# Performance work log

Measured on AMD Instinct MI355X. Metric: run time of the kernel, lower is better.

Reference implementation:

```python
import jax, jax.numpy as jnp
import numpy as np

# ---- static config (matches init_kwargs) ----
OC, IC, K, S, PAD = 128, 64, 3, 1, 1
M, T, R = 5, 8, 2.5            # ALSH m, table_size, LSH bucket width r
SPAN = K * K * IC              # kernel_span = 576


def setup_inputs() -> dict:
    key = jax.random.key(0)
    k1, k2, k3, k4 = jax.random.split(key, 4)
    # xavier_uniform on the (OC, SPAN) kernel matrix
    bound = float(np.sqrt(6.0 / (OC + SPAN)))
    kernels = jax.random.uniform(k1, (OC, SPAN), minval=-bound, maxval=bound, dtype=jnp.float32)
    a = jax.random.normal(k2, (SPAN + M,), dtype=jnp.float32)          # LSH projection
    b = jax.random.uniform(k3, (), minval=0.0, maxval=R, dtype=jnp.float32)  # LSH offset
    x = jax.random.normal(k4, (16, IC, 56, 56), dtype=jnp.float32)
    return {"x": x, "kernels": kernels, "a": a, "b": b, "mode": 0}


def _im2col(x):
    # [B, SPAN, H2, W2] with feature order (C, kh, kw)
    p = jax.lax.conv_general_dilated_patches(x, (K, K), (S, S), [(PAD, PAD), (PAD, PAD)])
    B, _, H2, W2 = p.shape
    # patch matrix [SPAN, B*H2*W2]
    return p.transpose(1, 0, 2, 3).reshape(SPAN, -1), B, H2, W2


def _bucket(h):
    # floor((h+b)/r); fmod table_size; abs  (matches torch .fmod_ then .abs_)
    return jnp.abs(jnp.fmod(h.astype(jnp.int32), T))


def reference(x, kernels, a, b, mode):
    patch_matr, B, H2, W2 = _im2col(x)            # [SPAN, N], N = B*H2*W2

    # ---- vote: hash every patch column with Q-augmentation (append m halves) ----
    v = a[:SPAN] @ patch_matr + 0.5 * jnp.sum(a[SPAN:])      # [N]
    votes = _bucket(jnp.floor((v + b) / R))
    counts = jnp.zeros((T,), jnp.int32).at[votes].add(1)
    bucket = jnp.argmax(counts)                               # most common bucket

    # ---- hash table: hash each kernel row with P-augmentation (norm powers) ----
    norms2 = jnp.sum(kernels * kernels, axis=1)               # ||k||^2, [OC]
    powers = jnp.stack([norms2 ** (2 ** i) for i in range(M)], axis=1)  # ||k||^{2,4,...,2^M}
    hk = kernels @ a[:SPAN] + powers @ a[SPAN:]               # [OC]
    kidx = _bucket(jnp.floor((hk + b) / R))                   # bucket of each kernel

    # ---- select kernels in the winning bucket; scale by |rows|/OC ----
    mask = (kidx == bucket).astype(x.dtype)                   # [OC]
    cnt = jnp.sum(mask)
    # original gathers the selected rows (variable oc); we scatter back to the
    # full OC channels (zeros for inactive kernels) for static shapes.
    # empty bucket -> dense conv with all kernels, no rescale.
    factor = jnp.where(cnt > 0, mask * (OC / jnp.maximum(cnt, 1.0)), jnp.ones_like(mask))

    out = (kernels * factor[:, None]) @ patch_matr            # [OC, N]
    out = out.reshape(OC, B, H2 * W2).transpose(1, 0, 2)
    return out.reshape(B, OC, H2, W2)
```

## Files before the change

### kernel.cpp

```cpp
#include <hip/hip_runtime.h>
#include <math.h>

#define IC 64
#define OC 128
#define HH 56
#define WW 56
#define BATCH 16
#define HP 58
#define HW (HH*WW)
#define NPIX (BATCH*HW)
#define SPAN 576
#define TSIZE 8
#define PADBLK 211
#define VBANDS 28
#define VBLOCKS (BATCH*VBANDS)
#define NBLK1 (PADBLK + VBLOCKS + OC)

typedef unsigned short ushort_t;
typedef unsigned int uint_t;
typedef __attribute__((ext_vector_type(8))) __bf16 bf16x8;
typedef __attribute__((ext_vector_type(4))) float f32x4;

__device__ __forceinline__ ushort_t bf16_rne(float f) {
  uint_t u = __builtin_bit_cast(uint_t, f);
  u += 0x7FFFu + ((u >> 16) & 1u);
  return (ushort_t)(u >> 16);
}

__global__ __launch_bounds__(256)
void prep_kernel(const float* __restrict__ x, const float* __restrict__ kernels,
                 const float* __restrict__ a, const float* __restrict__ bptr,
                 ushort_t* __restrict__ xpad, ushort_t* __restrict__ w2,
                 int* __restrict__ rbucket, int* __restrict__ hist_partial) {
  __shared__ float tl[224 * 9];
  __shared__ int hist[TSIZE];
  __shared__ float red0[256], red1[256];
  const int bx = blockIdx.x, t = threadIdx.x;

  if (bx < PADBLK) {
    int idx = bx * 256 + t;
    if (idx >= BATCH * HP * HP) return;
    int b = idx / (HP * HP);
    int rem = idx % (HP * HP);
    int y = rem / HP, xw = rem % HP;
    int h = y - 1, w = xw - 1;
    bool inb = ((unsigned)h < (unsigned)HH) && ((unsigned)w < (unsigned)WW);
    const float* src = x + (size_t)b * IC * HW + (inb ? h * WW + w : 0);
    uint_t* dst = (uint_t*)(xpad + (size_t)idx * IC);
    #pragma unroll
    for (int c2 = 0; c2 < IC / 2; ++c2) {
      float f0 = inb ? src[(2 * c2) * HW] : 0.0f;
      float f1 = inb ? src[(2 * c2 + 1) * HW] : 0.0f;
      dst[c2] = (uint_t)bf16_rne(f0) | ((uint_t)bf16_rne(f1) << 16);
    }
  } else if (bx < PADBLK + VBLOCKS) {
    const int vb = bx - PADBLK;
    const int b = vb / VBANDS, band = vb % VBANDS;
    const int r0 = band * 2;
    if (t < TSIZE) hist[t] = 0;
    if (t < 224) {
      int prow = r0 - 1 + t / 56;
      int col = t % 56;
      float t9[9] = {0, 0, 0, 0, 0, 0, 0, 0, 0};
      if ((unsigned)prow < (unsigned)HH) {
        const float* xb = x + (size_t)b * IC * HW + prow * WW + col;
        #pragma unroll
        for (int c = 0; c < IC; ++c) {
          float xv = xb[(size_t)c * HW];
          #pragma unroll
          for (int tap = 0; tap < 9; ++tap) t9[tap] += a[c * 9 + tap] * xv;
        }
      }
      #pragma unroll
      for (int tap = 0; tap < 9; ++tap) tl[t * 9 + tap] = t9[tap];
    }
    __syncthreads();
    if (t < 112) {
      int lr = t / 56;
      int col = t % 56;
      float v = 0.0f;
      #pragma unroll
      for (int kh = 0; kh < 3; ++kh) {
        int gr = r0 + lr - 1 + kh;
        #pragma unroll
        for (int kw = 0; kw < 3; ++kw) {
          int cc = col - 1 + kw;
          if ((unsigned)gr < (unsigned)HH && (unsigned)cc < (unsigned)WW)
            v += tl[((lr + kh) * 56 + cc) * 9 + (kh * 3 + kw)];
        }
      }
      float tail = 0.5f * (a[576] + a[577] + a[578] + a[579] + a[580]);
      int hi = (int)floorf((v + tail + bptr[0]) / 2.5f);
      int r = hi % TSIZE;
      if (r < 0) r = -r;
      atomicAdd(&hist[r], 1);
    }
    __syncthreads();
    if (t < TSIZE) hist_partial[vb * TSIZE + t] = hist[t];
  } else {
    const int r = bx - (PADBLK + VBLOCKS);
    const float* row = kernels + (size_t)r * SPAN;
    float d = 0.0f, n2 = 0.0f;
    #pragma unroll
    for (int k0 = 0; k0 < 3; ++k0) {
      int k = k0 * 256 + t;
      if (k < SPAN) { float kv = row[k]; d += kv * a[k]; n2 += kv * kv; }
    }
    red0[t] = d; red1[t] = n2;
    __syncthreads();
    for (int s = 128; s > 0; s >>= 1) {
      if (t < s) { red0[t] += red0[t + s]; red1[t] += red1[t + s]; }
      __syncthreads();
    }
    if (t == 0) {
      float hk = red0[0], p = red1[0];
      #pragma unroll
      for (int i = 0; i < 5; ++i) { hk += p * a[SPAN + i]; p = p * p; }
      int hi = (int)floorf((hk + bptr[0]) / 2.5f);
      int rr = hi % TSIZE;
      if (rr < 0) rr = -rr;
      rbucket[r] = rr;
    }
    #pragma unroll
    for (int j0 = 0; j0 < 3; ++j0) {
      int j = j0 * 256 + t;
      if (j < SPAN) {
        int tap = j >> 6, c = j & 63;
        w2[(size_t)r * SPAN + j] = bf16_rne(row[c * 9 + tap]);
      }
    }
  }
}

__global__ __launch_bounds__(256, 4)
void gemm_kernel(const ushort_t* __restrict__ w2, const ushort_t* __restrict__ xpad,
                 const int* __restrict__ hist_partial, const int* __restrict__ rbucket,
                 float* __restrict__ out) {
  __shared__ ushort_t As[128 * 64];
  __shared__ ushort_t Bs[64 * 64];
  __shared__ float factor_s[OC];
  __shared__ int counts_s[TSIZE];
  __shared__ int cnt_w[4];
  const int tid = threadIdx.x;
  const int wave = tid >> 6, lane = tid & 63;
  const int n0 = blockIdx.x * 64;
  const int wm = wave * 32;

  const int srow = lane >> 3;
  const int sch = (lane & 7) ^ srow;

  int agbase[4], bgbase[2];
  #pragma unroll
  for (int i = 0; i < 4; ++i) {
    int row = wm + i * 8 + srow;
    agbase[i] = row * SPAN + sch * 8;
  }
  #pragma unroll
  for (int i = 0; i < 2; ++i) {
    int brow = wave * 16 + i * 8 + srow;
    int n = n0 + brow;
    int b = n / HW;
    int rem = n % HW;
    int h = rem / WW, w = rem % WW;
    bgbase[i] = ((b * HP + h) * HP + w) * IC + sch * 8;
  }

  f32x4 acc[2][4] = {};

  for (int tap = 0; tap < 9; ++tap) {
    const int kh = tap / 3, kw = tap % 3;
    const int toffA = tap * 64;
    const int toffB = (kh * HP + kw) * IC;
    __syncthreads();
    #pragma unroll
    for (int i = 0; i < 4; ++i)
      __builtin_amdgcn_global_load_lds(
          (const __attribute__((address_space(1))) void*)(w2 + agbase[i] + toffA),
          (__attribute__((address_space(3))) void*)(As + (wm + i * 8) * 64), 16, 0, 0);
    #pragma unroll
    for (int i = 0; i < 2; ++i)
      __builtin_amdgcn_global_load_lds(
          (const __attribute__((address_space(1))) void*)(xpad + bgbase[i] + toffB),
          (__attribute__((address_space(3))) void*)(Bs + (wave * 16 + i * 8) * 64), 16, 0, 0);
    __syncthreads();
    #pragma unroll
    for (int kk = 0; kk < 2; ++kk) {
      const int jf = kk * 4 + (lane >> 4);
      bf16x8 af[2], bfr[4];
      #pragma unroll
      for (int m = 0; m < 2; ++m) {
        int row = wm + m * 16 + (lane & 15);
        int slot = row * 8 + (jf ^ (row & 7));
        af[m] = *(const bf16x8*)(As + slot * 8);
      }
      #pragma unroll
      for (int n = 0; n < 4; ++n) {
        int col = n * 16 + (lane & 15);
        int slot = col * 8 + (jf ^ (col & 7));
        bfr[n] = *(const bf16x8*)(Bs + slot * 8);
      }
      #pragma unroll
      for (int m = 0; m < 2; ++m)
        #pragma unroll
        for (int n = 0; n < 4; ++n)
          acc[m][n] = __builtin_amdgcn_mfma_f32_16x16x32_bf16(af[m], bfr[n], acc[m][n], 0, 0, 0);
    }
  }

  if (tid < TSIZE) counts_s[tid] = 0;
  __syncthreads();
  {
    int bin = tid >> 5;
    int s = 0;
    for (int k = (tid & 31); k < VBLOCKS; k += 32) s += hist_partial[k * TSIZE + bin];
    atomicAdd(&counts_s[bin], s);
  }
  __syncthreads();
  int best = counts_s[0], bi = 0;
  #pragma unroll
  for (int i = 1; i < TSIZE; ++i) { int c = counts_s[i]; if (c > best) { best = c; bi = i; } }
  int isin = (tid < OC) ? ((rbucket[tid] == bi) ? 1 : 0) : 0;
  unsigned long long bal = __ballot(isin != 0);
  if (lane == 0) cnt_w[wave] = __popcll(bal);
  __syncthreads();
  int cnt = cnt_w[0] + cnt_w[1] + cnt_w[2] + cnt_w[3];
  if (tid < OC)
    factor_s[tid] = (cnt > 0) ? (isin ? 128.0f / (float)cnt : 0.0f) : 1.0f;
  __syncthreads();

  #pragma unroll
  for (int n = 0; n < 4; ++n) {
    int np = n0 + n * 16 + (lane & 15);
    int b = np / HW;
    int rem = np % HW;
    float* obase = out + ((size_t)b * OC) * HW + rem;
    #pragma unroll
    for (int m = 0; m < 2; ++m) {
      int ocb = wm + m * 16 + (lane >> 4) * 4;
      #pragma unroll
      for (int r = 0; r < 4; ++r) {
        obase[(size_t)(ocb + r) * HW] = acc[m][n][r] * factor_s[ocb + r];
      }
    }
  }
}

extern "C" void kernel_launch(void* const* d_in, const int* in_sizes, int n_in,
                              void* d_out, int out_size, void* d_ws, size_t ws_size,
                              hipStream_t stream) {
  (void)in_sizes; (void)n_in; (void)out_size; (void)ws_size;
  const float* x = (const float*)d_in[0];
  const float* kernels = (const float*)d_in[1];
  const float* a = (const float*)d_in[2];
  const float* b = (const float*)d_in[3];
  float* out = (float*)d_out;

  char* ws = (char*)d_ws;
  int* rbucket = (int*)ws;
  int* hist_partial = (int*)(ws + 512);
  ushort_t* w2 = (ushort_t*)(ws + 16384);
  ushort_t* xpad = (ushort_t*)(ws + 16384 + 147456);

  prep_kernel<<<NBLK1, 256, 0, stream>>>(x, kernels, a, b, xpad, w2, rbucket, hist_partial);
  gemm_kernel<<<NPIX / 64, 256, 0, stream>>>(w2, xpad, hist_partial, rbucket, out);
}
```

Before: 109.2 us.

## Fuse bf16 padded-input conversion into vote blocks to reuse x reads

The separate padding/conversion blocks are removed. The vote blocks, which already read every x value for the LSH projection, now also round those values to bf16, stage them in shared memory and write the padded channel-last interior of xpad. A few new per-image blocks zero the padding border. This aims to avoid reading the fp32 input twice, at the cost of more work, more shared memory and uncoalesced-ish stores inside the vote blocks.

```diff
diff --git a/kernel.cpp b/kernel.cpp
--- a/kernel.cpp
+++ b/kernel.cpp
@@ -11,10 +11,11 @@
 #define NPIX (BATCH*HW)
 #define SPAN 576
 #define TSIZE 8
-#define PADBLK 211
 #define VBANDS 28
 #define VBLOCKS (BATCH*VBANDS)
-#define NBLK1 (PADBLK + VBLOCKS + OC)
+#define W2BASE  VBLOCKS
+#define BORDBASE (VBLOCKS + OC)
+#define NBLK1 (BORDBASE + BATCH)
 
 typedef unsigned short ushort_t;
 typedef unsigned int uint_t;
@@ -33,51 +34,36 @@
                  ushort_t* __restrict__ xpad, ushort_t* __restrict__ w2,
                  int* __restrict__ rbucket, int* __restrict__ hist_partial) {
   __shared__ float tl[224 * 9];
+  __shared__ ushort_t lx[112 * 66];
   __shared__ int hist[TSIZE];
   __shared__ float red0[256], red1[256];
   const int bx = blockIdx.x, t = threadIdx.x;
 
-  if (bx < PADBLK) {
-    int idx = bx * 256 + t;
-    if (idx >= BATCH * HP * HP) return;
-    int b = idx / (HP * HP);
-    int rem = idx % (HP * HP);
-    int y = rem / HP, xw = rem % HP;
-    int h = y - 1, w = xw - 1;
-    bool inb = ((unsigned)h < (unsigned)HH) && ((unsigned)w < (unsigned)WW);
-    const float* src = x + (size_t)b * IC * HW + (inb ? h * WW + w : 0);
-    uint_t* dst = (uint_t*)(xpad + (size_t)idx * IC);
-    #pragma unroll
-    for (int c2 = 0; c2 < IC / 2; ++c2) {
-      float f0 = inb ? src[(2 * c2) * HW] : 0.0f;
-      float f1 = inb ? src[(2 * c2 + 1) * HW] : 0.0f;
-      dst[c2] = (uint_t)bf16_rne(f0) | ((uint_t)bf16_rne(f1) << 16);
-    }
-  } else if (bx < PADBLK + VBLOCKS) {
-    const int vb = bx - PADBLK;
-    const int b = vb / VBANDS, band = vb % VBANDS;
+  if (bx < VBLOCKS) {
+    const int b = bx / VBANDS, band = bx % VBANDS;
     const int r0 = band * 2;
     if (t < TSIZE) hist[t] = 0;
     if (t < 224) {
-      int prow = r0 - 1 + t / 56;
-      int col = t % 56;
+      const int prow = r0 - 1 + t / 56;
+      const int col = t % 56;
+      const bool inr = ((unsigned)prow < (unsigned)HH);
+      const bool mid = (t >= 56 && t < 168);
+      const float* xb = x + (size_t)b * IC * HW + (inr ? prow * WW + col : 0);
+      ushort_t* lxp = lx + (mid ? (t - 56) : 0) * 66;
       float t9[9] = {0, 0, 0, 0, 0, 0, 0, 0, 0};
-      if ((unsigned)prow < (unsigned)HH) {
-        const float* xb = x + (size_t)b * IC * HW + prow * WW + col;
+      #pragma unroll 8
+      for (int c = 0; c < IC; ++c) {
+        float xv = inr ? xb[(size_t)c * HW] : 0.0f;
         #pragma unroll
-        for (int c = 0; c < IC; ++c) {
-          float xv = xb[(size_t)c * HW];
-          #pragma unroll
-          for (int tap = 0; tap < 9; ++tap) t9[tap] += a[c * 9 + tap] * xv;
-        }
+        for (int tap = 0; tap < 9; ++tap) t9[tap] += a[c * 9 + tap] * xv;
+        if (mid) lxp[c] = bf16_rne(xv);
       }
       #pragma unroll
       for (int tap = 0; tap < 9; ++tap) tl[t * 9 + tap] = t9[tap];
     }
     __syncthreads();
     if (t < 112) {
-      int lr = t / 56;
-      int col = t % 56;
+      int lr = t / 56, col = t % 56;
       float v = 0.0f;
       #pragma unroll
       for (int kh = 0; kh < 3; ++kh) {
@@ -95,10 +81,22 @@
       if (r < 0) r = -r;
       atomicAdd(&hist[r], 1);
     }
-    __syncthreads();
-    if (t < TSIZE) hist_partial[vb * TSIZE + t] = hist[t];
-  } else {
-    const int r = bx - (PADBLK + VBLOCKS);
+    {
+      const uint_t* lxu = (const uint_t*)lx;
+      uint_t* xp = (uint_t*)xpad;
+      #pragma unroll
+      for (int j = 0; j < 14; ++j) {
+        int idx = j * 256 + t;
+        int px = idx >> 5, cp = idx & 31;
+        int lr = px / 56, c0 = px % 56;
+        int y = r0 + 1 + lr, xw = c0 + 1;
+        xp[(((size_t)(b * HP + y)) * HP + xw) * 32 + cp] = lxu[px * 33 + cp];
+      }
+    }
+    __syncthreads();
+    if (t < TSIZE) hist_partial[bx * TSIZE + t] = hist[t];
+  } else if (bx < BORDBASE) {
+    const int r = bx - W2BASE;
     const float* row = kernels + (size_t)r * SPAN;
     float d = 0.0f, n2 = 0.0f;
     #pragma unroll
@@ -128,6 +126,17 @@
         int tap = j >> 6, c = j & 63;
         w2[(size_t)r * SPAN + j] = bf16_rne(row[c * 9 + tap]);
       }
+    }
+  } else {
+    const int ib = bx - BORDBASE;
+    uint_t* xp = (uint_t*)xpad + (size_t)ib * HP * HP * 32;
+    for (int j = t; j < 7296; j += 256) {
+      int px = j >> 5, cp = j & 31;
+      int y, xw;
+      if (px < 58) { y = 0; xw = px; }
+      else if (px < 116) { y = 57; xw = px - 58; }
+      else { int k = px - 116; y = 1 + (k >> 1); xw = (k & 1) * 57; }
+      xp[((size_t)y * HP + xw) * 32 + cp] = 0;
     }
   }
 }
```

New measurement: 112.3 us. +2.9%, slower.
